# Kernel optimization log

Measured on AMD Instinct MI355X. Metric: run time of the kernel, lower is better.

Reference implementation:

```python
import jax, jax.numpy as jnp
import numpy as np

B, N = 256, 128  # batch, n_neurons; n_equations = 4*N


def _pos(k, shape):
    # positive parameters (conductances, capacitance, time constants)
    return jax.random.uniform(k, shape, jnp.float32, 0.5, 1.5)


def setup_inputs() -> dict:
    key = jax.random.key(0)
    ks = jax.random.split(key, 17)
    return {
        "y": jax.random.normal(ks[0], (B, 4 * N), jnp.float32),
        "Ic": jax.random.normal(ks[1], (B,), jnp.float32),  # I(t) evaluated, per-batch current
        "C": _pos(ks[2], (N,)),
        "g_Na": _pos(ks[3], (N,)),
        "E_Na": jax.random.normal(ks[4], (N,), jnp.float32),
        "g_K": _pos(ks[5], (N,)),
        "E_K": jax.random.normal(ks[6], (N,), jnp.float32),
        "g_L": _pos(ks[7], (N,)),
        "E_L": jax.random.normal(ks[8], (N,), jnp.float32),
        "m_inf": jax.random.uniform(ks[9], (N,), jnp.float32),
        "tau_m": _pos(ks[10], (N,)),
        "h_inf": jax.random.uniform(ks[11], (N,), jnp.float32),
        "tau_h": _pos(ks[12], (N,)),
        "n_inf": jax.random.uniform(ks[13], (N,), jnp.float32),
        "tau_n": _pos(ks[14], (N,)),
        "g_C": 0.1 * _pos(ks[15], (N, N)),
    }


def _diag_embed(x):
    # x: (..., N) -> (..., N, N) with x on the diagonal
    return x[..., :, None] * jnp.eye(x.shape[-1], dtype=x.dtype)


def reference(y, Ic, C, g_Na, E_Na, g_K, E_K, g_L, E_L,
              m_inf, tau_m, h_inf, tau_h, n_inf, tau_n, g_C):
    V = y[..., 0::4]  # (B, N)
    m = y[..., 1::4]
    h = y[..., 2::4]
    n = y[..., 3::4]

    invC = 1.0 / C  # (N,)
    Vdot = invC * (-g_Na * m ** 3 * h * (V - E_Na)
                   - g_K * n ** 4 * (V - E_K)
                   - g_L * (V - E_L)
                   + Ic[..., None])
    # coupling: sum_j g_C[i,j] * (V_i - V_j) / C[j]  (C broadcasts over last axis, as in torch)
    dV = jnp.sum(g_C[None, :, :] * (V[..., :, None] - V[..., None, :]) * invC[None, None, :], axis=-1)
    Vdot = Vdot + dV
    mdot = (m_inf - m) / tau_m
    hdot = (h_inf - h) / tau_h
    ndot = (n_inf - n) / tau_n
    # interleave back to (B, 4N) matching y[..., 0::4] layout
    ydot = jnp.stack([Vdot, mdot, hdot, ndot], axis=-1).reshape(y.shape)

    E = y.shape[-1]
    J = jnp.zeros(y.shape + (E,), dtype=y.dtype)

    gC_over_C = g_C * invC[None, :]  # (N, N), column-wise division as in torch broadcast
    JVV = (_diag_embed(invC * (-g_L - g_Na * h * m ** 3 - g_K * n ** 4))
           - gC_over_C[None, :, :]
           + jnp.eye(N, dtype=y.dtype) * jnp.sum(gC_over_C))
    J = J.at[..., 0::4, 0::4].set(JVV)
    J = J.at[..., 0::4, 1::4].set(_diag_embed(-invC * (3.0 * g_Na * h * m ** 2 * (V - E_Na))))
    J = J.at[..., 0::4, 2::4].set(_diag_embed(-invC * (g_Na * m ** 3 * (V - E_Na))))
    J = J.at[..., 0::4, 3::4].set(_diag_embed(-invC * (4.0 * g_K * n ** 3 * (V - E_K))))
    J = J.at[..., 1::4, 1::4].set(jnp.diag(-1.0 / tau_m))
    J = J.at[..., 2::4, 2::4].set(jnp.diag(-1.0 / tau_h))
    J = J.at[..., 3::4, 3::4].set(jnp.diag(-1.0 / tau_n))

    return ydot, J
```

## Files before the change

### kernel.cpp

```cpp
#include <hip/hip_runtime.h>

#define BATCH 256
#define NN    128
#define EDIM  512
#define E4    128

typedef float vf4 __attribute__((ext_vector_type(4)));

__global__ __launch_bounds__(128) void hh_k1(
    const float* __restrict__ y,     const float* __restrict__ Ic,
    const float* __restrict__ C,     const float* __restrict__ g_Na,
    const float* __restrict__ E_Na,  const float* __restrict__ g_K,
    const float* __restrict__ E_K,   const float* __restrict__ g_L,
    const float* __restrict__ E_L,   const float* __restrict__ m_inf,
    const float* __restrict__ tau_m, const float* __restrict__ h_inf,
    const float* __restrict__ tau_h, const float* __restrict__ n_inf,
    const float* __restrict__ tau_n, const float* __restrict__ g_C,
    float* __restrict__ ydot_out,    float4* __restrict__ jtab,
    float* __restrict__ invC_out,    float* __restrict__ nitab)
{
    __shared__ float sInvC[NN];
    __shared__ float sW[NN];
    __shared__ float sRed[NN];

    const int b = blockIdx.x;
    const int i = threadIdx.x;

    const float4 yv = ((const float4*)(y + (size_t)b * EDIM))[i];
    const float V = yv.x, m = yv.y, h = yv.z, n = yv.w;

    const float invC = 1.0f / C[i];
    sInvC[i] = invC;
    sW[i]    = V * invC;
    __syncthreads();

    float rowS = 0.f, dotW = 0.f;
    const float4* grow = (const float4*)(g_C + i * NN);
#pragma unroll 8
    for (int j4 = 0; j4 < NN / 4; ++j4) {
        const float4 g = grow[j4];
        const int j = j4 * 4;
        rowS += g.x * sInvC[j] + g.y * sInvC[j + 1] + g.z * sInvC[j + 2] + g.w * sInvC[j + 3];
        dotW += g.x * sW[j]    + g.y * sW[j + 1]    + g.z * sW[j + 2]    + g.w * sW[j + 3];
    }
    const float dV = V * rowS - dotW;

    sRed[i] = rowS;
    __syncthreads();
    for (int s = NN / 2; s > 0; s >>= 1) {
        if (i < s) sRed[i] += sRed[i + s];
        __syncthreads();
    }
    const float S = sRed[0];

    const float m2 = m * m, m3 = m2 * m;
    const float n2 = n * n, n3 = n2 * n, n4 = n3 * n;
    const float gna = g_Na[i], ena = E_Na[i];
    const float gk  = g_K[i],  ek  = E_K[i];
    const float gl  = g_L[i],  el  = E_L[i];

    const float Vdot = invC * (-gna * m3 * h * (V - ena)
                               - gk * n4 * (V - ek)
                               - gl * (V - el)
                               + Ic[b]) + dV;
    const float itm = 1.0f / tau_m[i];
    const float ith = 1.0f / tau_h[i];
    const float itn = 1.0f / tau_n[i];
    const float mdot = (m_inf[i] - m) * itm;
    const float hdot = (h_inf[i] - h) * ith;
    const float ndot = (n_inf[i] - n) * itn;

    ((float4*)(ydot_out + (size_t)b * EDIM))[i] = make_float4(Vdot, mdot, hdot, ndot);

    const float jvv = invC * (-gl - gna * h * m3 - gk * n4) + S;
    const float jvm = -invC * (3.0f * gna * h * m2 * (V - ena));
    const float jvh = -invC * (gna * m3 * (V - ena));
    const float jvn = -invC * (4.0f * gk * n3 * (V - ek));
    jtab[(b << 7) + i] = make_float4(jvv, jvm, jvh, jvn);

    if (b == 0) {
        invC_out[i]        = invC;
        nitab[i]           = -itm;
        nitab[NN + i]      = -ith;
        nitab[2 * NN + i]  = -itn;
    }
}

__global__ __launch_bounds__(256) void hh_k2(
    const float4* __restrict__ jtab, const float* __restrict__ invC,
    const float* __restrict__ nitab, const float* __restrict__ g_C,
    vf4* __restrict__ J)
{
    const unsigned idx = blockIdx.x * 256u + threadIdx.x;
    const int c4      = idx & (E4 - 1);
    const unsigned rw = idx >> 7;
    const int r       = rw & (EDIM - 1);
    const int b       = rw >> 9;
    const int a       = r & 3;
    const int i       = r >> 2;

    float v0 = 0.f, v1 = 0.f, v2 = 0.f, v3 = 0.f;
    if (a == 0) {
        const float g = g_C[(i << 7) + c4];
        v0 = -g * invC[c4];
        if (c4 == i) {
            const float4 jv = jtab[(b << 7) + i];
            v0 += jv.x; v1 = jv.y; v2 = jv.z; v3 = jv.w;
        }
    } else if (c4 == i) {
        const float nit = nitab[((a - 1) << 7) + i];
        if (a == 1)      v1 = nit;
        else if (a == 2) v2 = nit;
        else             v3 = nit;
    }
    const vf4 v = {v0, v1, v2, v3};
    __builtin_nontemporal_store(v, &J[idx]);
}

extern "C" void kernel_launch(void* const* d_in, const int* in_sizes, int n_in,
                              void* d_out, int out_size, void* d_ws, size_t ws_size,
                              hipStream_t stream) {
    const float* y     = (const float*)d_in[0];
    const float* Ic    = (const float*)d_in[1];
    const float* C     = (const float*)d_in[2];
    const float* g_Na  = (const float*)d_in[3];
    const float* E_Na  = (const float*)d_in[4];
    const float* g_K   = (const float*)d_in[5];
    const float* E_K   = (const float*)d_in[6];
    const float* g_L   = (const float*)d_in[7];
    const float* E_L   = (const float*)d_in[8];
    const float* m_inf = (const float*)d_in[9];
    const float* tau_m = (const float*)d_in[10];
    const float* h_inf = (const float*)d_in[11];
    const float* tau_h = (const float*)d_in[12];
    const float* n_inf = (const float*)d_in[13];
    const float* tau_n = (const float*)d_in[14];
    const float* g_C   = (const float*)d_in[15];

    float* ydot = (float*)d_out;
    vf4*   J    = (vf4*)((float*)d_out + (size_t)BATCH * EDIM);

    float4* jtab = (float4*)d_ws;
    float*  invC = (float*)((char*)d_ws + (size_t)BATCH * NN * sizeof(float4));
    float*  nit  = invC + NN;

    hh_k1<<<BATCH, NN, 0, stream>>>(y, Ic, C, g_Na, E_Na, g_K, E_K, g_L, E_L,
                                    m_inf, tau_m, h_inf, tau_h, n_inf, tau_n,
                                    g_C, ydot, jtab, invC, nit);

    const unsigned total4 = (unsigned)BATCH * EDIM * E4;
    hh_k2<<<total4 / 256, 256, 0, stream>>>(jtab, invC, nit, g_C, J);
}
```

Baseline: 294.5 us.

## Split k1 rows across 4 threads and reorganize k2 by row-type groups

The first kernel now runs 512 threads per batch, so four threads share each row's g_C dot products. Partial sums are combined with wave shuffles, and the tree reduction becomes a single-wave shuffle reduction. The Jacobian kernel gives each 32-thread group one whole output row, ordered by row type (a = 0..3), which removes per-element divergence and index math. It also drops the nontemporal store hint, which may change how the 128 MB write interacts with the cache.

```diff
diff --git a/kernel.cpp b/kernel.cpp
--- a/kernel.cpp
+++ b/kernel.cpp
@@ -3,11 +3,10 @@
 #define BATCH 256
 #define NN    128
 #define EDIM  512
-#define E4    128
 
 typedef float vf4 __attribute__((ext_vector_type(4)));
 
-__global__ __launch_bounds__(128) void hh_k1(
+__global__ __launch_bounds__(512) void hh_k1(
     const float* __restrict__ y,     const float* __restrict__ Ic,
     const float* __restrict__ C,     const float* __restrict__ g_Na,
     const float* __restrict__ E_Na,  const float* __restrict__ g_K,
@@ -22,67 +21,79 @@
     __shared__ float sInvC[NN];
     __shared__ float sW[NN];
     __shared__ float sRed[NN];
+    __shared__ float sS;
 
-    const int b = blockIdx.x;
-    const int i = threadIdx.x;
+    const int b  = blockIdx.x;
+    const int t  = threadIdx.x;
+    const int i  = t >> 2;
+    const int jq = t & 3;
 
-    const float4 yv = ((const float4*)(y + (size_t)b * EDIM))[i];
-    const float V = yv.x, m = yv.y, h = yv.z, n = yv.w;
-
-    const float invC = 1.0f / C[i];
-    sInvC[i] = invC;
-    sW[i]    = V * invC;
+    if (t < NN) {
+        const float ic = 1.0f / C[t];
+        sInvC[t] = ic;
+        sW[t] = y[(size_t)b * EDIM + 4 * t] * ic;
+    }
     __syncthreads();
 
     float rowS = 0.f, dotW = 0.f;
-    const float4* grow = (const float4*)(g_C + i * NN);
-#pragma unroll 8
-    for (int j4 = 0; j4 < NN / 4; ++j4) {
+    const float4* grow = (const float4*)(g_C + (i << 7) + (jq << 5));
+#pragma unroll
+    for (int j4 = 0; j4 < 8; ++j4) {
         const float4 g = grow[j4];
-        const int j = j4 * 4;
+        const int j = (jq << 5) + j4 * 4;
         rowS += g.x * sInvC[j] + g.y * sInvC[j + 1] + g.z * sInvC[j + 2] + g.w * sInvC[j + 3];
         dotW += g.x * sW[j]    + g.y * sW[j + 1]    + g.z * sW[j + 2]    + g.w * sW[j + 3];
     }
-    const float dV = V * rowS - dotW;
+    rowS += __shfl_xor(rowS, 1);  rowS += __shfl_xor(rowS, 2);
+    dotW += __shfl_xor(dotW, 1);  dotW += __shfl_xor(dotW, 2);
 
-    sRed[i] = rowS;
+    if (jq == 0) sRed[i] = rowS;
     __syncthreads();
-    for (int s = NN / 2; s > 0; s >>= 1) {
-        if (i < s) sRed[i] += sRed[i + s];
-        __syncthreads();
+    if (t < 64) {
+        float v = sRed[t] + sRed[t + 64];
+        v += __shfl_xor(v, 1);  v += __shfl_xor(v, 2);  v += __shfl_xor(v, 4);
+        v += __shfl_xor(v, 8);  v += __shfl_xor(v, 16); v += __shfl_xor(v, 32);
+        if (t == 0) sS = v;
     }
-    const float S = sRed[0];
+    __syncthreads();
 
-    const float m2 = m * m, m3 = m2 * m;
-    const float n2 = n * n, n3 = n2 * n, n4 = n3 * n;
-    const float gna = g_Na[i], ena = E_Na[i];
-    const float gk  = g_K[i],  ek  = E_K[i];
-    const float gl  = g_L[i],  el  = E_L[i];
+    if (jq == 0) {
+        const float S = sS;
+        const float4 yv = ((const float4*)(y + (size_t)b * EDIM))[i];
+        const float V = yv.x, m = yv.y, h = yv.z, n = yv.w;
+        const float invC = sInvC[i];
+        const float dV = V * rowS - dotW;
 
-    const float Vdot = invC * (-gna * m3 * h * (V - ena)
-                               - gk * n4 * (V - ek)
-                               - gl * (V - el)
-                               + Ic[b]) + dV;
-    const float itm = 1.0f / tau_m[i];
-    const float ith = 1.0f / tau_h[i];
-    const float itn = 1.0f / tau_n[i];
-    const float mdot = (m_inf[i] - m) * itm;
-    const float hdot = (h_inf[i] - h) * ith;
-    const float ndot = (n_inf[i] - n) * itn;
+        const float m2 = m * m, m3 = m2 * m;
+        const float n2 = n * n, n3 = n2 * n, n4 = n3 * n;
+        const float gna = g_Na[i], ena = E_Na[i];
+        const float gk  = g_K[i],  ek  = E_K[i];
+        const float gl  = g_L[i],  el  = E_L[i];
 
-    ((float4*)(ydot_out + (size_t)b * EDIM))[i] = make_float4(Vdot, mdot, hdot, ndot);
+        const float Vdot = invC * (-gna * m3 * h * (V - ena)
+                                   - gk * n4 * (V - ek)
+                                   - gl * (V - el)
+                                   + Ic[b]) + dV;
+        const float itm = 1.0f / tau_m[i];
+        const float ith = 1.0f / tau_h[i];
+        const float itn = 1.0f / tau_n[i];
 
-    const float jvv = invC * (-gl - gna * h * m3 - gk * n4) + S;
-    const float jvm = -invC * (3.0f * gna * h * m2 * (V - ena));
-    const float jvh = -invC * (gna * m3 * (V - ena));
-    const float jvn = -invC * (4.0f * gk * n3 * (V - ek));
-    jtab[(b << 7) + i] = make_float4(jvv, jvm, jvh, jvn);
+        ((float4*)(ydot_out + (size_t)b * EDIM))[i] =
+            make_float4(Vdot, (m_inf[i] - m) * itm, (h_inf[i] - h) * ith,
+                        (n_inf[i] - n) * itn);
 
-    if (b == 0) {
-        invC_out[i]        = invC;
-        nitab[i]           = -itm;
-        nitab[NN + i]      = -ith;
-        nitab[2 * NN + i]  = -itn;
+        const float jvv = invC * (-gl - gna * h * m3 - gk * n4) + S;
+        const float jvm = -invC * (3.0f * gna * h * m2 * (V - ena));
+        const float jvh = -invC * (gna * m3 * (V - ena));
+        const float jvn = -invC * (4.0f * gk * n3 * (V - ek));
+        jtab[(b << 7) + i] = make_float4(jvv, jvm, jvh, jvn);
+
+        if (b == 0) {
+            invC_out[i]       = invC;
+            nitab[i]          = -itm;
+            nitab[NN + i]     = -ith;
+            nitab[2 * NN + i] = -itn;
+        }
     }
 }
 
@@ -91,30 +102,42 @@
     const float* __restrict__ nitab, const float* __restrict__ g_C,
     vf4* __restrict__ J)
 {
-    const unsigned idx = blockIdx.x * 256u + threadIdx.x;
-    const int c4      = idx & (E4 - 1);
-    const unsigned rw = idx >> 7;
-    const int r       = rw & (EDIM - 1);
-    const int b       = rw >> 9;
-    const int a       = r & 3;
-    const int i       = r >> 2;
+    const int t = threadIdx.x;
+    const int q = t & 31;
+    const unsigned g = blockIdx.x * 8u + (t >> 5);
+    const int a = g >> 15;
+    const unsigned s = g & 32767u;
+    const int b = s >> 7;
+    const int i = s & 127;
+    const unsigned row = ((unsigned)b << 9) | ((unsigned)i << 2) | (unsigned)a;
 
-    float v0 = 0.f, v1 = 0.f, v2 = 0.f, v3 = 0.f;
+    vf4* __restrict__ Jrow = J + (size_t)row * 128;
+
     if (a == 0) {
-        const float g = g_C[(i << 7) + c4];
-        v0 = -g * invC[c4];
-        if (c4 == i) {
-            const float4 jv = jtab[(b << 7) + i];
-            v0 += jv.x; v1 = jv.y; v2 = jv.z; v3 = jv.w;
+        const float4 jv = jtab[(b << 7) + i];
+#pragma unroll
+        for (int k = 0; k < 4; ++k) {
+            const int j = q + 32 * k;
+            float v0 = -g_C[(i << 7) + j] * invC[j];
+            float v1 = 0.f, v2 = 0.f, v3 = 0.f;
+            if (j == i) { v0 += jv.x; v1 = jv.y; v2 = jv.z; v3 = jv.w; }
+            const vf4 v = {v0, v1, v2, v3};
+            Jrow[j] = v;
         }
-    } else if (c4 == i) {
+    } else {
         const float nit = nitab[((a - 1) << 7) + i];
-        if (a == 1)      v1 = nit;
-        else if (a == 2) v2 = nit;
-        else             v3 = nit;
+#pragma unroll
+        for (int k = 0; k < 4; ++k) {
+            const int j = q + 32 * k;
+            vf4 v = {0.f, 0.f, 0.f, 0.f};
+            if (j == i) {
+                if (a == 1)      v.y = nit;
+                else if (a == 2) v.z = nit;
+                else             v.w = nit;
+            }
+            Jrow[j] = v;
+        }
     }
-    const vf4 v = {v0, v1, v2, v3};
-    __builtin_nontemporal_store(v, &J[idx]);
 }
 
 extern "C" void kernel_launch(void* const* d_in, const int* in_sizes, int n_in,
@@ -144,10 +167,9 @@
     float*  invC = (float*)((char*)d_ws + (size_t)BATCH * NN * sizeof(float4));
     float*  nit  = invC + NN;
 
-    hh_k1<<<BATCH, NN, 0, stream>>>(y, Ic, C, g_Na, E_Na, g_K, E_K, g_L, E_L,
-                                    m_inf, tau_m, h_inf, tau_h, n_inf, tau_n,
-                                    g_C, ydot, jtab, invC, nit);
+    hh_k1<<<BATCH, 512, 0, stream>>>(y, Ic, C, g_Na, E_Na, g_K, E_K, g_L, E_L,
+                                     m_inf, tau_m, h_inf, tau_h, n_inf, tau_n,
+                                     g_C, ydot, jtab, invC, nit);
 
-    const unsigned total4 = (unsigned)BATCH * EDIM * E4;
-    hh_k2<<<total4 / 256, 256, 0, stream>>>(jtab, invC, nit, g_C, J);
+    hh_k2<<<131072 / 8, 256, 0, stream>>>(jtab, invC, nit, g_C, J);
 }
```

After: 287.4 us. 2.4% less time.
